# Optimization experiments

Hardware: AMD Instinct MI355X
Metric: run time of the kernel (lower is better)

The kernel has to match this reference:

```python
import jax, jax.numpy as jnp
import numpy as np

LN_EPS = 1e-5


def setup_inputs() -> dict:
    key = jax.random.key(0)
    k1, k2, k3 = jax.random.split(key, 3)
    B, E, IN, OUT = 16384, 8, 1024, 1024
    w_bound = (6.0 / (IN * OUT)) ** 0.5
    x = jax.random.normal(k1, (B, IN), dtype=jnp.float32)
    coef = jax.random.uniform(k2, (B, E), dtype=jnp.float32)
    w = jax.random.uniform(k3, (E, OUT, IN), dtype=jnp.float32,
                           minval=-w_bound, maxval=w_bound)
    b = jnp.zeros((E, OUT), dtype=jnp.float32)
    gamma = jnp.ones((OUT,), dtype=jnp.float32)
    beta = jnp.zeros((OUT,), dtype=jnp.float32)
    return {"x": x, "coef": coef, "w": w, "b": b, "gamma": gamma, "beta": beta}


def reference(x, coef, w, b, gamma, beta):
    # Soft-MoE linear: algebraically identical to the torch einsum chain
    #   w_b = einsum('be,ejk->bjk'); y = einsum('bk,bjk->bj') + einsum('be,ek->bk')
    # Reordered to avoid materializing [B,out,in]:
    #   per-expert projections [B,E,out], then coef-weighted combine.
    y = jnp.einsum('bk,ejk->bej', x, w)          # [B, E, out]
    y = jnp.einsum('be,bej->bj', coef, y)        # [B, out]
    y = y + coef @ b                              # [B, out]
    # LayerNorm(out_channels)
    mu = jnp.mean(y, axis=-1, keepdims=True)
    var = jnp.mean(jnp.square(y - mu), axis=-1, keepdims=True)
    y = (y - mu) * jax.lax.rsqrt(var + LN_EPS) * gamma + beta
    # GELU (torch nn.GELU default = exact erf form)
    y = jax.nn.gelu(y, approximate=False)
    return y
```

## Files before the change

kernel.cpp:

```cpp
#include <hip/hip_runtime.h>
#include <hip/hip_bf16.h>


typedef __attribute__((ext_vector_type(8))) short bf16x8;
typedef __attribute__((ext_vector_type(16))) float f32x16;

__device__ __forceinline__ unsigned short f2bf_rn(float f) {
    union { float f; unsigned u; } v; v.f = f;
    unsigned r = v.u + 0x7FFFu + ((v.u >> 16) & 1u);
    return (unsigned short)(r >> 16);
}
__device__ __forceinline__ float bf2f(unsigned short h) {
    union { unsigned u; float f; } v; v.u = ((unsigned)h) << 16; return v.f;
}

__global__ __launch_bounds__(256) void split_f32_bf16(
        const float* __restrict__ in, unsigned short* __restrict__ hi,
        unsigned short* __restrict__ lo, int n4) {
    int i = blockIdx.x * blockDim.x + threadIdx.x;
    const int stride = gridDim.x * blockDim.x;
    for (; i < n4; i += stride) {
        float4 v = ((const float4*)in)[i];
        ushort4 h, l;
        h.x = f2bf_rn(v.x); l.x = f2bf_rn(v.x - bf2f(h.x));
        h.y = f2bf_rn(v.y); l.y = f2bf_rn(v.y - bf2f(h.y));
        h.z = f2bf_rn(v.z); l.z = f2bf_rn(v.z - bf2f(h.z));
        h.w = f2bf_rn(v.w); l.w = f2bf_rn(v.w - bf2f(h.w));
        ((ushort4*)hi)[i] = h;
        ((ushort4*)lo)[i] = l;
    }
}

#define BUF_USH 24576

#define GLD(gp, lp) __builtin_amdgcn_global_load_lds( \
    (const __attribute__((address_space(1))) void*)(gp), \
    (__attribute__((address_space(3))) void*)(lp), 16, 0, 0)

__global__ __launch_bounds__(512, 2) void gemm_moe(
        const unsigned short* __restrict__ xh, const unsigned short* __restrict__ xl,
        const unsigned short* __restrict__ wh, const unsigned short* __restrict__ wl,
        const float* __restrict__ coef, float* __restrict__ y) {
    __shared__ unsigned short S[3 * BUF_USH];
    __shared__ float coef_s[2048];

    const int bid = blockIdx.x;
    const int nb = bid & 7;
    const int mb = bid >> 3;
    const int m0 = mb * 256, n0 = nb * 128;
    const int t = threadIdx.x;
    const int lane = t & 63;
    const int wid = t >> 6;
    const int wm = wid >> 1, wn = wid & 1;
    const int lr = lane & 31, hi = lane >> 5;

    ((float4*)coef_s)[t] = ((const float4*)(coef + (size_t)m0 * 8))[t];
    __syncthreads();

    const int ar = t >> 2;
    const int acs = (t & 3) ^ ((ar >> 1) & 3);
    const unsigned short* agh = xh + (size_t)(m0 + ar) * 1024 + acs * 8;
    const unsigned short* agl = xl + (size_t)(m0 + ar) * 1024 + acs * 8;
    const size_t bofs = (size_t)(n0 + ar) * 1024 + acs * 8;
    const unsigned short* wgh = wh + bofs;
    const unsigned short* wgl = wl + bofs;

    int aoff[2][2], boff[2][2];
#pragma unroll
    for (int i = 0; i < 2; ++i)
#pragma unroll
        for (int s = 0; s < 2; ++s) {
            const int slot = ((s << 1) + hi) ^ ((lr >> 1) & 3);
            aoff[i][s] = (wm * 64 + i * 32 + lr) * 32 + slot * 8;
            boff[i][s] = (wn * 64 + i * 32 + lr) * 32 + slot * 8;
        }

    f32x16 acc[2][2] = {};
    f32x16 acc_t[2][2] = {};

    auto STAGE = [&](int kt2, int bufi) {
        unsigned short* bp = S + bufi * BUF_USH;
        const size_t eo = (size_t)(kt2 >> 5) << 20;
        const int ko = (kt2 & 31) << 5;
        GLD(agh + ko,           bp + t * 8);
        GLD(agh + 131072 + ko,  bp + 4096 + t * 8);
        GLD(agl + ko,           bp + 8192 + t * 8);
        GLD(agl + 131072 + ko,  bp + 12288 + t * 8);
        GLD(wgh + eo + ko,      bp + 16384 + t * 8);
        GLD(wgl + eo + ko,      bp + 20480 + t * 8);
    };

    STAGE(0, 0);
    STAGE(1, 1);
    asm volatile("s_waitcnt vmcnt(6)" ::: "memory");
    __builtin_amdgcn_s_barrier();

    int cur = 0;
#pragma unroll 1
    for (int kt = 0; kt < 256; ++kt) {
        const unsigned short* bp = S + cur * BUF_USH;
        bf16x8 ah[2][2], al[2][2], bh2[2][2], bl2[2][2];
#pragma unroll
        for (int i = 0; i < 2; ++i)
#pragma unroll
            for (int s = 0; s < 2; ++s) {
                ah[i][s]  = *(const bf16x8*)(bp + aoff[i][s]);
                al[i][s]  = *(const bf16x8*)(bp + 8192 + aoff[i][s]);
                bh2[i][s] = *(const bf16x8*)(bp + 16384 + boff[i][s]);
                bl2[i][s] = *(const bf16x8*)(bp + 20480 + boff[i][s]);
            }
        if (kt < 254) {
            int stg = cur + 2; if (stg >= 3) stg -= 3;
            STAGE(kt + 2, stg);
        }

        __builtin_amdgcn_s_setprio(1);
#pragma unroll
        for (int s = 0; s < 2; ++s)
#pragma unroll
            for (int i = 0; i < 2; ++i)
#pragma unroll
                for (int j = 0; j < 2; ++j) {
                    acc[i][j] = __builtin_amdgcn_mfma_f32_32x32x16_bf16(
                        ah[i][s], bh2[j][s], acc[i][j], 0, 0, 0);
                    acc[i][j] = __builtin_amdgcn_mfma_f32_32x32x16_bf16(
                        ah[i][s], bl2[j][s], acc[i][j], 0, 0, 0);
                    acc[i][j] = __builtin_amdgcn_mfma_f32_32x32x16_bf16(
                        al[i][s], bh2[j][s], acc[i][j], 0, 0, 0);
                }
        __builtin_amdgcn_s_setprio(0);

        if ((kt & 31) == 31) {
            const int e = kt >> 5;
#pragma unroll
            for (int i = 0; i < 2; ++i)
#pragma unroll
                for (int r = 0; r < 16; ++r) {
                    const int row = wm * 64 + i * 32 + (r & 3) + 8 * (r >> 2) + 4 * hi;
                    const float c = coef_s[row * 8 + e];
                    acc_t[i][0][r] += c * acc[i][0][r]; acc[i][0][r] = 0.f;
                    acc_t[i][1][r] += c * acc[i][1][r]; acc[i][1][r] = 0.f;
                }
        }

        if (kt < 254) asm volatile("s_waitcnt vmcnt(6)" ::: "memory");
        else          asm volatile("s_waitcnt vmcnt(0)" ::: "memory");
        __builtin_amdgcn_s_barrier();
        cur = (cur == 2) ? 0 : cur + 1;
    }

#pragma unroll
    for (int i = 0; i < 2; ++i)
#pragma unroll
        for (int j = 0; j < 2; ++j) {
            const int n = n0 + wn * 64 + j * 32 + lr;
#pragma unroll
            for (int r = 0; r < 16; ++r) {
                const int m = m0 + wm * 64 + i * 32 + (r & 3) + 8 * (r >> 2) + 4 * hi;
                y[(size_t)m * 1024 + n] = acc_t[i][j][r];
            }
        }
}

__global__ __launch_bounds__(256) void ln_gelu(
        const float* __restrict__ y, const float* __restrict__ coef,
        const float* __restrict__ bexp, const float* __restrict__ gamma,
        const float* __restrict__ beta, float* __restrict__ out) {
    const int b = blockIdx.x;
    const int t = threadIdx.x;
    float4 v = ((const float4*)(y + (size_t)b * 1024))[t];

    float c[8];
#pragma unroll
    for (int e = 0; e < 8; ++e) c[e] = coef[(size_t)b * 8 + e];
    float bx = 0.f, by = 0.f, bz = 0.f, bw = 0.f;
#pragma unroll
    for (int e = 0; e < 8; ++e) {
        float4 w4 = ((const float4*)(bexp + (size_t)e * 1024))[t];
        bx += c[e] * w4.x; by += c[e] * w4.y;
        bz += c[e] * w4.z; bw += c[e] * w4.w;
    }
    v.x += bx; v.y += by; v.z += bz; v.w += bw;

    float s = v.x + v.y + v.z + v.w;
    float s2 = v.x * v.x + v.y * v.y + v.z * v.z + v.w * v.w;
#pragma unroll
    for (int off = 32; off >= 1; off >>= 1) {
        s  += __shfl_xor(s,  off);
        s2 += __shfl_xor(s2, off);
    }
    __shared__ float red[8];
    const int lane = t & 63, w = t >> 6;
    if (lane == 0) { red[w] = s; red[4 + w] = s2; }
    __syncthreads();
    s  = red[0] + red[1] + red[2] + red[3];
    s2 = red[4] + red[5] + red[6] + red[7];

    const float mu = s * (1.0f / 1024.0f);
    const float var = s2 * (1.0f / 1024.0f) - mu * mu;
    const float rstd = rsqrtf(var + 1e-5f);
    float4 g = ((const float4*)gamma)[t];
    float4 be = ((const float4*)beta)[t];
    float4 o;
    {
        float yy = (v.x - mu) * rstd * g.x + be.x;
        o.x = 0.5f * yy * (1.0f + erff(yy * 0.70710678118654752f));
        yy = (v.y - mu) * rstd * g.y + be.y;
        o.y = 0.5f * yy * (1.0f + erff(yy * 0.70710678118654752f));
        yy = (v.z - mu) * rstd * g.z + be.z;
        o.z = 0.5f * yy * (1.0f + erff(yy * 0.70710678118654752f));
        yy = (v.w - mu) * rstd * g.w + be.w;
        o.w = 0.5f * yy * (1.0f + erff(yy * 0.70710678118654752f));
    }
    ((float4*)(out + (size_t)b * 1024))[t] = o;
}

extern "C" void kernel_launch(void* const* d_in, const int* in_sizes, int n_in,
                              void* d_out, int out_size, void* d_ws, size_t ws_size,
                              hipStream_t stream) {
    (void)in_sizes; (void)n_in; (void)out_size; (void)ws_size;
    const float* x     = (const float*)d_in[0];
    const float* coef  = (const float*)d_in[1];
    const float* w     = (const float*)d_in[2];
    const float* bexp  = (const float*)d_in[3];
    const float* gamma = (const float*)d_in[4];
    const float* beta  = (const float*)d_in[5];
    float* out = (float*)d_out;

    unsigned short* xh = (unsigned short*)d_ws;
    unsigned short* xl = xh + 16777216;
    unsigned short* wh = xl + 16777216;
    unsigned short* wl = wh + 8388608;
    float* ymid = (float*)(wl + 8388608);

    split_f32_bf16<<<2048, 256, 0, stream>>>(x, xh, xl, 16777216 / 4);
    split_f32_bf16<<<1024, 256, 0, stream>>>(w, wh, wl, 8388608 / 4);
    gemm_moe<<<512, 512, 0, stream>>>(xh, xl, wh, wl, coef, ymid);
    ln_gelu<<<16384, 256, 0, stream>>>(ymid, coef, bexp, gamma, beta, out);
}
```

Baseline: 969.9 us.

## Fold coef into per-expert scaled x copies and run one long-K GEMM

```diff
diff --git a/kernel.cpp b/kernel.cpp
--- a/kernel.cpp
+++ b/kernel.cpp
@@ -13,6 +13,10 @@
 __device__ __forceinline__ float bf2f(unsigned short h) {
     union { unsigned u; float f; } v; v.u = ((unsigned)h) << 16; return v.f;
 }
+
+#define GLD(gp, lp) __builtin_amdgcn_global_load_lds( \
+    (const __attribute__((address_space(1))) void*)(gp), \
+    (__attribute__((address_space(3))) void*)(lp), 16, 0, 0)
 
 __global__ __launch_bounds__(256) void split_f32_bf16(
         const float* __restrict__ in, unsigned short* __restrict__ hi,
@@ -31,11 +35,138 @@
     }
 }
 
+__global__ __launch_bounds__(256) void scale_split(
+        const float* __restrict__ x, const float* __restrict__ coef,
+        unsigned short* __restrict__ xs_h, unsigned short* __restrict__ xs_l) {
+    const int b = blockIdx.x;
+    const int t = threadIdx.x;
+    float4 v = ((const float4*)(x + (size_t)b * 1024))[t];
+    float c8[8];
+#pragma unroll
+    for (int e = 0; e < 8; ++e) c8[e] = coef[(size_t)b * 8 + e];
+#pragma unroll
+    for (int e = 0; e < 8; ++e) {
+        float4 p;
+        p.x = c8[e] * v.x; p.y = c8[e] * v.y;
+        p.z = c8[e] * v.z; p.w = c8[e] * v.w;
+        ushort4 h, l;
+        h.x = f2bf_rn(p.x); l.x = f2bf_rn(p.x - bf2f(h.x));
+        h.y = f2bf_rn(p.y); l.y = f2bf_rn(p.y - bf2f(h.y));
+        h.z = f2bf_rn(p.z); l.z = f2bf_rn(p.z - bf2f(h.z));
+        h.w = f2bf_rn(p.w); l.w = f2bf_rn(p.w - bf2f(h.w));
+        const size_t base = (size_t)e * 16777216 + (size_t)b * 1024;
+        ((ushort4*)(xs_h + base))[t] = h;
+        ((ushort4*)(xs_l + base))[t] = l;
+    }
+}
+
+__global__ __launch_bounds__(512, 2) void gemm_moe_fast(
+        const unsigned short* __restrict__ xs_h, const unsigned short* __restrict__ xs_l,
+        const unsigned short* __restrict__ wh, const unsigned short* __restrict__ wl,
+        float* __restrict__ y) {
+    __shared__ unsigned short S[2 * 32768];
+
+    const int bid = blockIdx.x;
+    const int nb = (bid & 7) >> 1;
+    const int mb = ((bid >> 3) << 1) | (bid & 1);
+    const int m0 = mb * 256, n0 = nb * 256;
+    const int t = threadIdx.x;
+    const int lane = t & 63;
+    const int wid = t >> 6;
+    const int wm = wid >> 2, wn = wid & 3;
+    const int lr = lane & 31, hi = lane >> 5;
+
+    const int ar = t >> 2;
+    const int acs = (t & 3) ^ ((ar >> 1) & 3);
+    const unsigned short* agh = xs_h + (size_t)(m0 + ar) * 1024 + acs * 8;
+    const unsigned short* agl = xs_l + (size_t)(m0 + ar) * 1024 + acs * 8;
+    const unsigned short* bgh = wh + (size_t)(n0 + ar) * 1024 + acs * 8;
+    const unsigned short* bgl = wl + (size_t)(n0 + ar) * 1024 + acs * 8;
+
+    int aoff[4][2], boff[2][2];
+#pragma unroll
+    for (int s = 0; s < 2; ++s) {
+        const int slot = (((s << 1) + hi) ^ ((lr >> 1) & 3)) * 8;
+#pragma unroll
+        for (int i = 0; i < 4; ++i)
+            aoff[i][s] = (wm * 128 + i * 32 + lr) * 32 + slot;
+#pragma unroll
+        for (int j = 0; j < 2; ++j)
+            boff[j][s] = (wn * 64 + j * 32 + lr) * 32 + slot;
+    }
+
+    f32x16 acc[4][2] = {};
+
+    auto STAGE = [&](int kt) {
+        unsigned short* bp = S + (kt & 1) * 32768;
+        const size_t ea = (size_t)(kt >> 5) * 16777216;
+        const size_t eb = (size_t)(kt >> 5) * 1048576;
+        const int ko = (kt & 31) << 5;
+        GLD(agh + ea + ko,           bp + t * 8);
+        GLD(agh + ea + 131072 + ko,  bp + 4096 + t * 8);
+        GLD(agl + ea + ko,           bp + 8192 + t * 8);
+        GLD(agl + ea + 131072 + ko,  bp + 12288 + t * 8);
+        GLD(bgh + eb + ko,           bp + 16384 + t * 8);
+        GLD(bgh + eb + 131072 + ko,  bp + 20480 + t * 8);
+        GLD(bgl + eb + ko,           bp + 24576 + t * 8);
+        GLD(bgl + eb + 131072 + ko,  bp + 28672 + t * 8);
+    };
+
+    STAGE(0);
+    asm volatile("s_waitcnt vmcnt(0)" ::: "memory");
+    __builtin_amdgcn_s_barrier();
+
+#pragma unroll 1
+    for (int kt = 0; kt < 256; ++kt) {
+        const unsigned short* bp = S + (kt & 1) * 32768;
+        if (kt < 255) STAGE(kt + 1);
+#pragma unroll
+        for (int s = 0; s < 2; ++s) {
+            bf16x8 ah[4], al[4], bh2[2], bl2[2];
+#pragma unroll
+            for (int i = 0; i < 4; ++i) {
+                ah[i] = *(const bf16x8*)(bp + aoff[i][s]);
+                al[i] = *(const bf16x8*)(bp + 8192 + aoff[i][s]);
+            }
+#pragma unroll
+            for (int j = 0; j < 2; ++j) {
+                bh2[j] = *(const bf16x8*)(bp + 16384 + boff[j][s]);
+                bl2[j] = *(const bf16x8*)(bp + 24576 + boff[j][s]);
+            }
+            __builtin_amdgcn_s_setprio(1);
+#pragma unroll
+            for (int i = 0; i < 4; ++i)
+#pragma unroll
+                for (int j = 0; j < 2; ++j) {
+                    acc[i][j] = __builtin_amdgcn_mfma_f32_32x32x16_bf16(
+                        ah[i], bh2[j], acc[i][j], 0, 0, 0);
+                    acc[i][j] = __builtin_amdgcn_mfma_f32_32x32x16_bf16(
+                        ah[i], bl2[j], acc[i][j], 0, 0, 0);
+                    acc[i][j] = __builtin_amdgcn_mfma_f32_32x32x16_bf16(
+                        al[i], bh2[j], acc[i][j], 0, 0, 0);
+                }
+            __builtin_amdgcn_s_setprio(0);
+        }
+        if (kt < 255) {
+            asm volatile("s_waitcnt vmcnt(0)" ::: "memory");
+            __builtin_amdgcn_s_barrier();
+        }
+    }
+
+#pragma unroll
+    for (int i = 0; i < 4; ++i)
+#pragma unroll
+        for (int j = 0; j < 2; ++j) {
+            const int n = n0 + wn * 64 + j * 32 + lr;
+#pragma unroll
+            for (int r = 0; r < 16; ++r) {
+                const int m = m0 + wm * 128 + i * 32 + (r & 3) + 8 * (r >> 2) + 4 * hi;
+                y[(size_t)m * 1024 + n] = acc[i][j][r];
+            }
+        }
+}
+
 #define BUF_USH 24576
-
-#define GLD(gp, lp) __builtin_amdgcn_global_load_lds( \
-    (const __attribute__((address_space(1))) void*)(gp), \
-    (__attribute__((address_space(3))) void*)(lp), 16, 0, 0)
 
 __global__ __launch_bounds__(512, 2) void gemm_moe(
         const unsigned short* __restrict__ xh, const unsigned short* __restrict__ xl,
@@ -82,12 +213,12 @@
         unsigned short* bp = S + bufi * BUF_USH;
         const size_t eo = (size_t)(kt2 >> 5) << 20;
         const int ko = (kt2 & 31) << 5;
-        GLD(agh + ko,           bp + t * 8);
-        GLD(agh + 131072 + ko,  bp + 4096 + t * 8);
-        GLD(agl + ko,           bp + 8192 + t * 8);
-        GLD(agl + 131072 + ko,  bp + 12288 + t * 8);
-        GLD(wgh + eo + ko,      bp + 16384 + t * 8);
-        GLD(wgl + eo + ko,      bp + 20480 + t * 8);
+        GLD(agh + ko,          bp + t * 8);
+        GLD(agh + 131072 + ko, bp + 4096 + t * 8);
+        GLD(agl + ko,          bp + 8192 + t * 8);
+        GLD(agl + 131072 + ko, bp + 12288 + t * 8);
+        GLD(wgh + eo + ko,     bp + 16384 + t * 8);
+        GLD(wgl + eo + ko,     bp + 20480 + t * 8);
     };
 
     STAGE(0, 0);
@@ -218,7 +349,7 @@
 extern "C" void kernel_launch(void* const* d_in, const int* in_sizes, int n_in,
                               void* d_out, int out_size, void* d_ws, size_t ws_size,
                               hipStream_t stream) {
-    (void)in_sizes; (void)n_in; (void)out_size; (void)ws_size;
+    (void)in_sizes; (void)n_in; (void)out_size;
     const float* x     = (const float*)d_in[0];
     const float* coef  = (const float*)d_in[1];
     const float* w     = (const float*)d_in[2];
@@ -227,14 +358,28 @@
     const float* beta  = (const float*)d_in[5];
     float* out = (float*)d_out;
 
-    unsigned short* xh = (unsigned short*)d_ws;
-    unsigned short* xl = xh + 16777216;
-    unsigned short* wh = xl + 16777216;
-    unsigned short* wl = wh + 8388608;
-    float* ymid = (float*)(wl + 8388608);
-
-    split_f32_bf16<<<2048, 256, 0, stream>>>(x, xh, xl, 16777216 / 4);
-    split_f32_bf16<<<1024, 256, 0, stream>>>(w, wh, wl, 8388608 / 4);
-    gemm_moe<<<512, 512, 0, stream>>>(xh, xl, wh, wl, coef, ymid);
-    ln_gelu<<<16384, 256, 0, stream>>>(ymid, coef, bexp, gamma, beta, out);
-}
+    const size_t NEED_FAST = 637534208ull;
+    if (ws_size >= NEED_FAST) {
+        unsigned short* xs_h = (unsigned short*)d_ws;
+        unsigned short* xs_l = xs_h + 134217728;
+        unsigned short* wh   = xs_l + 134217728;
+        unsigned short* wl   = wh + 8388608;
+        float* ymid = (float*)(wl + 8388608);
+
+        scale_split<<<16384, 256, 0, stream>>>(x, coef, xs_h, xs_l);
+        split_f32_bf16<<<1024, 256, 0, stream>>>(w, wh, wl, 8388608 / 4);
+        gemm_moe_fast<<<256, 512, 0, stream>>>(xs_h, xs_l, wh, wl, ymid);
+        ln_gelu<<<16384, 256, 0, stream>>>(ymid, coef, bexp, gamma, beta, out);
+    } else {
+        unsigned short* xh = (unsigned short*)d_ws;
+        unsigned short* xl = xh + 16777216;
+        unsigned short* wh = xl + 16777216;
+        unsigned short* wl = wh + 8388608;
+        float* ymid = (float*)(wl + 8388608);
+
+        split_f32_bf16<<<2048, 256, 0, stream>>>(x, xh, xl, 16777216 / 4);
+        split_f32_bf16<<<1024, 256, 0, stream>>>(w, wh, wl, 8388608 / 4);
+        gemm_moe<<<512, 512, 0, stream>>>(xh, xl, wh, wl, coef, ymid);
+        ln_gelu<<<16384, 256, 0, stream>>>(ymid, coef, bexp, gamma, beta, out);
+    }
+}
```

Result: slower. 1.003 ms (+3.4%).
